# Kernel tuning notes

Measured on AMD Instinct MI355X. Metric: run time of the kernel, lower is better.

## Reference

```python
import jax, jax.numpy as jnp
import numpy as np

N_NODES = 50000
N_EDGES = 800000
N_GRAPHS = 500
DIM = 64
RBF_DIM = 5      # ceil(cutoff/width) = ceil(5.0/1)
N_CONV = 3
N_TYPES = 100
CLS_DIM = 2000
CUTOFF = 5.0

def _w(key, shape, fan_in):
    return jax.random.normal(key, shape, dtype=jnp.float32) / np.sqrt(fan_in)

def setup_inputs() -> dict:
    key = jax.random.key(0)
    ks = jax.random.split(key, 16)
    return {
        "node_types": jax.random.randint(ks[0], (N_NODES,), 0, N_TYPES, dtype=jnp.int32),
        "edge_src": jax.random.randint(ks[1], (N_EDGES,), 0, N_NODES, dtype=jnp.int32),
        "edge_dst": jax.random.randint(ks[2], (N_EDGES,), 0, N_NODES, dtype=jnp.int32),
        "graph_ids": jnp.sort(jax.random.randint(ks[3], (N_NODES,), 0, N_GRAPHS, dtype=jnp.int32)),
        "distance": jax.random.uniform(ks[4], (N_EDGES,), dtype=jnp.float32) * CUTOFF,
        "emb": jax.random.normal(ks[5], (N_TYPES, DIM), dtype=jnp.float32),
        "conv_w1": _w(ks[6], (N_CONV, DIM, DIM), DIM),
        "cf1_w": _w(ks[7], (N_CONV, RBF_DIM, DIM), RBF_DIM),
        "cf1_b": jnp.zeros((N_CONV, DIM), jnp.float32),
        "cf2_w": _w(ks[8], (N_CONV, DIM, DIM), DIM),
        "cf2_b": jnp.zeros((N_CONV, DIM), jnp.float32),
        "nl2_w": _w(ks[9], (N_CONV, DIM, DIM), DIM),
        "nl2_b": jnp.zeros((N_CONV, DIM), jnp.float32),
        "nl3_w": _w(ks[10], (N_CONV, DIM, DIM), DIM),
        "nl3_b": jnp.zeros((N_CONV, DIM), jnp.float32),
        "d1_w": _w(ks[11], (DIM, 256), DIM),
        "d1_b": jnp.zeros((256,), jnp.float32),
        "d2_w": _w(ks[12], (256, 256), 256),
        "d2_b": jnp.zeros((256,), jnp.float32),
        "cls_w": _w(ks[13], (256, CLS_DIM), 256),
        "cls_b": jnp.zeros((CLS_DIM,), jnp.float32),
        "ac_w": _w(ks[14], (256, N_TYPES), 256),
        "ac_b": jnp.zeros((N_TYPES,), jnp.float32),
    }

def _sp2(x):
    # torch nn.Softplus(beta=0.5): (1/0.5) * log(1 + exp(0.5 * x))
    return 2.0 * jax.nn.softplus(0.5 * x)

def reference(node_types, edge_src, edge_dst, graph_ids, distance, emb,
              conv_w1, cf1_w, cf1_b, cf2_w, cf2_b, nl2_w, nl2_b, nl3_w, nl3_b,
              d1_w, d1_b, d2_w, d2_b, cls_w, cls_b, ac_w, ac_b):
    # RBF expansion of edge distances: centers = linspace(low, high, n_centers)
    centers = jnp.linspace(0.0, CUTOFF, RBF_DIM)
    gap = centers[1] - centers[0]
    rbf = jnp.exp(-(1.0 / gap) * (distance[:, None] - centers) ** 2)  # [E, RBF_DIM]

    node = emb[node_types]                                            # AtomEmbedding -> [N, D]
    for i in range(N_CONV):                                           # Interaction layers
        new_node = node @ conv_w1[i]                                  # Linear(dim, dim, bias=False)
        eh = _sp2(rbf @ cf1_w[i] + cf1_b[i])                          # CFConv filter network
        eh = _sp2(eh @ cf2_w[i] + cf2_b[i])                           # [E, D]
        msg = new_node[edge_src] * eh                                 # fn.u_mul_e gather
        agg = jax.ops.segment_sum(msg, edge_dst, num_segments=N_NODES)  # fn.sum scatter
        t = _sp2(agg @ nl2_w[i] + nl2_b[i])
        node = node + t @ nl3_w[i] + nl3_b[i]                         # residual update

    atom = node @ d1_w + d1_b
    atom = jax.nn.softplus(atom) - jnp.log(2.0)                       # ShiftSoftplus
    res = atom @ d2_w + d2_b                                          # [N, 256]
    atoms_preds = jax.nn.relu(res) @ ac_w + ac_b                      # [N, 100]

    ones = jnp.ones((N_NODES,), jnp.float32)
    counts = jax.ops.segment_sum(ones, graph_ids, num_segments=N_GRAPHS)
    emb_g = jax.ops.segment_sum(res, graph_ids, num_segments=N_GRAPHS) / jnp.maximum(counts, 1.0)[:, None]
    cls_preds = emb_g @ cls_w + cls_b                                 # [B, cls_dim]
    return atoms_preds, cls_preds
```

## Files before the change

### kernel.cpp

```cpp
#include <hip/hip_runtime.h>
#include <math.h>

#define N_NODES 50000
#define N_EDGES 800000
#define N_GRAPHS 500
#define DIM 64
#define RBF_DIM 5
#define N_CONV 3
#define CLS_DIM 2000
#define ACT_DIM 100
#define HID 256
#define TAB 2048
#define CAP 64

typedef __attribute__((ext_vector_type(8))) short bf16x8;
typedef __attribute__((ext_vector_type(4))) float f32x4;
#define MFMA16(a,b,c) __builtin_amdgcn_mfma_f32_16x16x32_bf16(a,b,c,0,0,0)

__device__ __forceinline__ float sp2f(float x){
    float y = 0.5f * x;
    return 2.0f * (fmaxf(y, 0.0f) + log1pf(__expf(-fabsf(y))));
}
__device__ __forceinline__ float sspf(float x){
    return fmaxf(x, 0.0f) + log1pf(__expf(-fabsf(x))) - 0.69314718055994531f;
}
__device__ __forceinline__ short f2b(float x){
    union { float f; unsigned u; } v; v.f = x;
    unsigned r = v.u + 0x7FFFu + ((v.u >> 16) & 1u);
    return (short)(r >> 16);
}
__device__ __forceinline__ float b2f(short x){
    union { unsigned u; float f; } v; v.u = ((unsigned)(unsigned short)x) << 16;
    return v.f;
}

__global__ void k_tw(const float* __restrict__ cw, const float* __restrict__ n2,
                     const float* __restrict__ n3, const float* __restrict__ d1w,
                     const float* __restrict__ d2w, const float* __restrict__ acw,
                     const float* __restrict__ clsw, const float* __restrict__ emb,
                     short* __restrict__ cwt, short* __restrict__ n2t, short* __restrict__ n3t,
                     short* __restrict__ d1t, short* __restrict__ d2t, short* __restrict__ act,
                     short* __restrict__ clswt, short* __restrict__ embw0b){
    int b = blockIdx.x, tid = threadIdx.x;
    if (b < 144){
        int i = b * 256 + tid;
        int y = i >> 12, j = i & 4095;
        int which = y / 3, layer = y % 3;
        const float* src = (which == 0 ? cw : which == 1 ? n2 : n3) + layer * 4096;
        short* dst = (which == 0 ? cwt : which == 1 ? n2t : n3t) + layer * 4096;
        int k = j >> 6, n = j & 63;
        dst[n * 64 + k] = f2b(src[k * 64 + n]);
    } else if (b < 208){
        int i = (b - 144) * 256 + tid;
        int k = i >> 8, n = i & 255;
        d1t[n * 64 + k] = f2b(d1w[k * 256 + n]);
    } else if (b < 464){
        int i = (b - 208) * 256 + tid;
        int k = i >> 8, n = i & 255;
        d2t[n * 256 + k] = f2b(d2w[k * 256 + n]);
    } else if (b < 576){
        int i = (b - 464) * 256 + tid;
        int n = i >> 8, k = i & 255;
        act[n * 256 + k] = f2b(n < ACT_DIM ? acw[k * ACT_DIM + n] : 0.f);
    } else if (b < 2624){
        int i = (b - 576) * 256 + tid;
        int k = i >> 11, n = i & 2047;
        clswt[n * 256 + k] = f2b(n < CLS_DIM ? clsw[k * CLS_DIM + n] : 0.f);
    } else {
        int i = (b - 2624) * 256 + tid;
        if (i < 100 * 64){
            int t = i >> 6, c = i & 63;
            float a = 0.f;
            #pragma unroll 8
            for (int k = 0; k < 64; ++k) a += emb[t * 64 + k] * cw[k * 64 + c];
            embw0b[i] = f2b(a);
        }
    }
}

__global__ void k_embed(const int* __restrict__ types, const float* __restrict__ emb,
                        const short* __restrict__ embw0b,
                        float* __restrict__ node, short* __restrict__ nodeb,
                        short* __restrict__ nnb,
                        const int* __restrict__ gid, float* __restrict__ counts,
                        const int* __restrict__ esrc, const int* __restrict__ edst,
                        const float* __restrict__ dist,
                        int* __restrict__ cnt, unsigned* __restrict__ edata){
    int i = blockIdx.x * 256 + threadIdx.x;
    if (i < N_NODES * DIM){
        int t = types[i >> 6], c = i & 63;
        float v = emb[t * 64 + c];
        node[i] = v; nodeb[i] = f2b(v);
        nnb[i] = embw0b[t * 64 + c];
    }
    if (i < N_EDGES){
        int d = edst[i];
        int pos = atomicAdd(&cnt[d], 1);
        if (pos < CAP){
            const float SC16 = (float)(TAB - 1) * 16.0f / 5.0f;
            int v = (int)(dist[i] * SC16 + 0.5f);
            v = min(v, 32767);
            edata[pos * N_NODES + d] = ((unsigned)v << 17) | (unsigned)esrc[i];
        }
    }
    if (i < N_NODES) atomicAdd(&counts[gid[i]], 1.0f);
}

__global__ __launch_bounds__(256) void k_table3(const float* __restrict__ cf1w_all,
    const float* __restrict__ cf1b_all, const float* __restrict__ cf2w_all,
    const float* __restrict__ cf2b_all, short* __restrict__ tabb_all)
{
    int L = blockIdx.y;
    const float* cf1w = cf1w_all + L * RBF_DIM * DIM;
    const float* cf1b = cf1b_all + L * DIM;
    const float* cf2w = cf2w_all + L * DIM * DIM;
    const float* cf2b = cf2b_all + L * DIM;
    short* tabb = tabb_all + L * TAB * 64;
    __shared__ float s_cf1[RBF_DIM * 64];
    __shared__ float s_cf1b[64], s_cf2b[64];
    __shared__ float s_cf2[64 * 64];
    __shared__ float s_h1[4 * 64];
    int tid = threadIdx.x;
    int c = tid & 63, g = tid >> 6;
    for (int i = tid; i < 64 * 64; i += 256) s_cf2[i] = cf2w[i];
    for (int i = tid; i < RBF_DIM * 64; i += 256) s_cf1[i] = cf1w[i];
    if (tid < 64){ s_cf1b[tid] = cf1b[tid]; s_cf2b[tid] = cf2b[tid]; }
    __syncthreads();
    int entry = blockIdx.x * 4 + g;
    float d = (float)entry * (5.0f / (float)(TAB - 1));
    {
        float acc = s_cf1b[c];
        #pragma unroll
        for (int j = 0; j < RBF_DIM; ++j){
            float t = d - 1.25f * (float)j;
            acc += __expf(-0.8f * t * t) * s_cf1[j * 64 + c];
        }
        s_h1[g * 64 + c] = sp2f(acc);
    }
    __syncthreads();
    {
        float acc = s_cf2b[c];
        #pragma unroll 8
        for (int k = 0; k < 64; ++k) acc += s_h1[g * 64 + k] * s_cf2[k * 64 + c];
        tabb[entry * 64 + c] = f2b(sp2f(acc));
    }
}

__global__ void k_pack(const short* __restrict__ tabb_all, unsigned* __restrict__ tabp_all){
    int L = blockIdx.y;
    int i = blockIdx.x * 256 + threadIdx.x;
    if (i < (TAB - 1) * 64){
        int t = i >> 6, c = i & 63;
        unsigned lo = (unsigned short)tabb_all[L * TAB * 64 + t * 64 + c];
        unsigned hi = (unsigned short)tabb_all[L * TAB * 64 + (t + 1) * 64 + c];
        tabp_all[L * TAB * 64 + t * 64 + c] = lo | (hi << 16);
    }
}

__global__ __launch_bounds__(256) void k_agg(const unsigned* __restrict__ edata,
    const int* __restrict__ cnt, const unsigned* __restrict__ tabp,
    const short* __restrict__ nnb, short* __restrict__ aggb)
{
    int tid = threadIdx.x;
    int c = tid & 63, r = tid >> 6;
    int n = blockIdx.x * 4 + r;
    if (n >= N_NODES) return;
    int m = min(cnt[n], CAP);
    unsigned ev = (c < m) ? edata[(long)c * N_NODES + n] : 0u;
    int s_l = (int)(ev & 0x1FFFFu);
    int v_l = (int)(ev >> 17);
    int i0_l = min(v_l >> 4, TAB - 2);
    float f_l = (float)(v_l - (i0_l << 4)) * 0.0625f;
    int pk_l = (i0_l << 17) | s_l;
    float acc = 0.f;
    int e = 0;
    for (; e + 4 <= m; e += 4){
        int   pa = __shfl(pk_l, e);     float fa = __shfl(f_l, e);
        int   pb = __shfl(pk_l, e + 1); float fb = __shfl(f_l, e + 1);
        int   pc = __shfl(pk_l, e + 2); float fc = __shfl(f_l, e + 2);
        int   pd = __shfl(pk_l, e + 3); float fd = __shfl(f_l, e + 3);
        int ia = pa >> 17, sa = pa & 0x1FFFF;
        int ib = pb >> 17, sb = pb & 0x1FFFF;
        int ic = pc >> 17, sc = pc & 0x1FFFF;
        int id = pd >> 17, sd = pd & 0x1FFFF;
        unsigned ua = tabp[ia * 64 + c], ub = tabp[ib * 64 + c];
        unsigned uc = tabp[ic * 64 + c], ud = tabp[id * 64 + c];
        float na = b2f(nnb[sa * 64 + c]), nb = b2f(nnb[sb * 64 + c]);
        float nc = b2f(nnb[sc * 64 + c]), nd = b2f(nnb[sd * 64 + c]);
        float wa0 = __uint_as_float(ua << 16), wa1 = __uint_as_float(ua & 0xffff0000u);
        float wb0 = __uint_as_float(ub << 16), wb1 = __uint_as_float(ub & 0xffff0000u);
        float wc0 = __uint_as_float(uc << 16), wc1 = __uint_as_float(uc & 0xffff0000u);
        float wd0 = __uint_as_float(ud << 16), wd1 = __uint_as_float(ud & 0xffff0000u);
        acc += na * (wa0 + (wa1 - wa0) * fa);
        acc += nb * (wb0 + (wb1 - wb0) * fb);
        acc += nc * (wc0 + (wc1 - wc0) * fc);
        acc += nd * (wd0 + (wd1 - wd0) * fd);
    }
    for (; e < m; ++e){
        int   p = __shfl(pk_l, e); float f = __shfl(f_l, e);
        int i0 = p >> 17, s = p & 0x1FFFF;
        unsigned u = tabp[i0 * 64 + c];
        float w0 = __uint_as_float(u << 16), w1 = __uint_as_float(u & 0xffff0000u);
        acc += b2f(nnb[s * 64 + c]) * (w0 + (w1 - w0) * f);
    }
    aggb[n * 64 + c] = f2b(acc);
}

__global__ __launch_bounds__(256) void k_update(const short* __restrict__ aggb,
    const short* __restrict__ nl2t, const float* __restrict__ nl2b,
    const short* __restrict__ nl3t, const float* __restrict__ nl3b,
    float* __restrict__ node, short* __restrict__ nodeb,
    const short* __restrict__ wnext, short* __restrict__ nnb)
{
    __shared__ short sT[32 * 80];
    int tid = threadIdx.x, wave = tid >> 6, lane = tid & 63;
    int quad = lane >> 4, l16 = lane & 15;
    int row0 = blockIdx.x * 32;
    int rt = wave >> 1;
    int ctb = (wave & 1) * 2;
    f32x4 acc[2] = {{0,0,0,0},{0,0,0,0}};
    #pragma unroll
    for (int kt = 0; kt < 2; ++kt){
        int k0 = kt * 32 + quad * 8;
        int rw = row0 + rt * 16 + l16;
        bf16x8 a = (rw < N_NODES) ? *(const bf16x8*)&aggb[rw * 64 + k0] : (bf16x8){0,0,0,0,0,0,0,0};
        #pragma unroll
        for (int i = 0; i < 2; ++i){
            bf16x8 b = *(const bf16x8*)&nl2t[((ctb + i) * 16 + l16) * 64 + k0];
            acc[i] = MFMA16(a, b, acc[i]);
        }
    }
    #pragma unroll
    for (int i = 0; i < 2; ++i)
        #pragma unroll
        for (int reg = 0; reg < 4; ++reg){
            int rl = rt * 16 + quad * 4 + reg;
            int col = (ctb + i) * 16 + l16;
            sT[rl * 80 + col] = f2b(sp2f(acc[i][reg] + nl2b[col]));
        }
    __syncthreads();
    f32x4 acc2[2] = {{0,0,0,0},{0,0,0,0}};
    #pragma unroll
    for (int kt = 0; kt < 2; ++kt){
        int k0 = kt * 32 + quad * 8;
        bf16x8 a = *(const bf16x8*)&sT[(rt * 16 + l16) * 80 + k0];
        #pragma unroll
        for (int i = 0; i < 2; ++i){
            bf16x8 b = *(const bf16x8*)&nl3t[((ctb + i) * 16 + l16) * 64 + k0];
            acc2[i] = MFMA16(a, b, acc2[i]);
        }
    }
    short vb[2][4];
    #pragma unroll
    for (int i = 0; i < 2; ++i)
        #pragma unroll
        for (int reg = 0; reg < 4; ++reg){
            int row = row0 + rt * 16 + quad * 4 + reg;
            int col = (ctb + i) * 16 + l16;
            float v = 0.f;
            if (row < N_NODES){
                v = node[row * 64 + col] + acc2[i][reg] + nl3b[col];
                node[row * 64 + col] = v;
            }
            short vbs = f2b(v);
            vb[i][reg] = vbs;
            if (row < N_NODES) nodeb[row * 64 + col] = vbs;
        }
    if (wnext){
        __syncthreads();
        #pragma unroll
        for (int i = 0; i < 2; ++i)
            #pragma unroll
            for (int reg = 0; reg < 4; ++reg)
                sT[(rt * 16 + quad * 4 + reg) * 80 + (ctb + i) * 16 + l16] = vb[i][reg];
        __syncthreads();
        f32x4 acc3[2] = {{0,0,0,0},{0,0,0,0}};
        #pragma unroll
        for (int kt = 0; kt < 2; ++kt){
            int k0 = kt * 32 + quad * 8;
            bf16x8 a = *(const bf16x8*)&sT[(rt * 16 + l16) * 80 + k0];
            #pragma unroll
            for (int i = 0; i < 2; ++i){
                bf16x8 b = *(const bf16x8*)&wnext[((ctb + i) * 16 + l16) * 64 + k0];
                acc3[i] = MFMA16(a, b, acc3[i]);
            }
        }
        #pragma unroll
        for (int i = 0; i < 2; ++i)
            #pragma unroll
            for (int reg = 0; reg < 4; ++reg){
                int row = row0 + rt * 16 + quad * 4 + reg;
                int col = (ctb + i) * 16 + l16;
                if (row < N_NODES) nnb[row * 64 + col] = f2b(acc3[i][reg]);
            }
    }
}

__global__ __launch_bounds__(256) void k_r1(const short* __restrict__ nodeb,
    const short* __restrict__ d1t, const float* __restrict__ d1b,
    short* __restrict__ atomb)
{
    int tid = threadIdx.x, wave = tid >> 6, lane = tid & 63;
    int quad = lane >> 4, l16 = lane & 15;
    int row0 = blockIdx.x * 32;
    f32x4 acc[2][4] = {{{0,0,0,0},{0,0,0,0},{0,0,0,0},{0,0,0,0}},
                       {{0,0,0,0},{0,0,0,0},{0,0,0,0},{0,0,0,0}}};
    #pragma unroll
    for (int kt = 0; kt < 2; ++kt){
        int k0 = kt * 32 + quad * 8;
        bf16x8 a[2];
        #pragma unroll
        for (int rt = 0; rt < 2; ++rt){
            int rw = row0 + rt * 16 + l16;
            a[rt] = (rw < N_NODES) ? *(const bf16x8*)&nodeb[rw * 64 + k0] : (bf16x8){0,0,0,0,0,0,0,0};
        }
        #pragma unroll
        for (int ct = 0; ct < 4; ++ct){
            int n = wave * 64 + ct * 16 + l16;
            bf16x8 b = *(const bf16x8*)&d1t[n * 64 + k0];
            #pragma unroll
            for (int rt = 0; rt < 2; ++rt) acc[rt][ct] = MFMA16(a[rt], b, acc[rt][ct]);
        }
    }
    #pragma unroll
    for (int rt = 0; rt < 2; ++rt)
        #pragma unroll
        for (int ct = 0; ct < 4; ++ct){
            int col = wave * 64 + ct * 16 + l16;
            float bb = d1b[col];
            #pragma unroll
            for (int reg = 0; reg < 4; ++reg){
                int row = row0 + rt * 16 + quad * 4 + reg;
                if (row < N_NODES) atomb[row * HID + col] = f2b(sspf(acc[rt][ct][reg] + bb));
            }
        }
}

__global__ __launch_bounds__(256) void k_r2(const short* __restrict__ atomb,
    const short* __restrict__ d2t, const float* __restrict__ d2b_,
    const int* __restrict__ gid, float* __restrict__ gacc, short* __restrict__ resb)
{
    __shared__ float sres[32 * 260];
    int tid = threadIdx.x, wave = tid >> 6, lane = tid & 63;
    int quad = lane >> 4, l16 = lane & 15;
    int row0 = blockIdx.x * 32;
    f32x4 acc[2][4] = {{{0,0,0,0},{0,0,0,0},{0,0,0,0},{0,0,0,0}},
                       {{0,0,0,0},{0,0,0,0},{0,0,0,0},{0,0,0,0}}};
    for (int kt = 0; kt < 8; ++kt){
        int k0 = kt * 32 + quad * 8;
        bf16x8 a[2];
        #pragma unroll
        for (int rt = 0; rt < 2; ++rt){
            int rw = row0 + rt * 16 + l16;
            a[rt] = (rw < N_NODES) ? *(const bf16x8*)&atomb[rw * HID + k0] : (bf16x8){0,0,0,0,0,0,0,0};
        }
        #pragma unroll
        for (int ct = 0; ct < 4; ++ct){
            int n = wave * 64 + ct * 16 + l16;
            bf16x8 b = *(const bf16x8*)&d2t[n * HID + k0];
            #pragma unroll
            for (int rt = 0; rt < 2; ++rt) acc[rt][ct] = MFMA16(a[rt], b, acc[rt][ct]);
        }
    }
    #pragma unroll
    for (int rt = 0; rt < 2; ++rt)
        #pragma unroll
        for (int ct = 0; ct < 4; ++ct){
            int col = wave * 64 + ct * 16 + l16;
            float bb = d2b_[col];
            #pragma unroll
            for (int reg = 0; reg < 4; ++reg){
                int rl = rt * 16 + quad * 4 + reg;
                sres[rl * 260 + col] = acc[rt][ct][reg] + bb;
            }
        }
    __syncthreads();
    float run = 0.f; int cur = -1;
    for (int r = 0; r < 32; ++r){
        int n = row0 + r;
        if (n >= N_NODES) break;
        float v = sres[r * 260 + tid];
        int g = gid[n];
        if (g != cur){
            if (cur >= 0) atomicAdd(&gacc[cur * HID + tid], run);
            run = 0.f; cur = g;
        }
        run += v;
        resb[n * HID + tid] = f2b(fmaxf(v, 0.f));
    }
    if (cur >= 0) atomicAdd(&gacc[cur * HID + tid], run);
}

__global__ __launch_bounds__(256) void k_r3(const short* __restrict__ resb,
    const short* __restrict__ act, const float* __restrict__ acb,
    float* __restrict__ out_atoms)
{
    int tid = threadIdx.x, wave = tid >> 6, lane = tid & 63;
    int quad = lane >> 4, l16 = lane & 15;
    int row0 = blockIdx.x * 64;
    f32x4 acc[7] = {{0,0,0,0},{0,0,0,0},{0,0,0,0},{0,0,0,0},{0,0,0,0},{0,0,0,0},{0,0,0,0}};
    for (int kt = 0; kt < 8; ++kt){
        int k0 = kt * 32 + quad * 8;
        int rw = row0 + wave * 16 + l16;
        bf16x8 a = (rw < N_NODES) ? *(const bf16x8*)&resb[rw * HID + k0] : (bf16x8){0,0,0,0,0,0,0,0};
        #pragma unroll
        for (int ct = 0; ct < 7; ++ct){
            bf16x8 b = *(const bf16x8*)&act[(ct * 16 + l16) * HID + k0];
            acc[ct] = MFMA16(a, b, acc[ct]);
        }
    }
    #pragma unroll
    for (int ct = 0; ct < 7; ++ct){
        int col = ct * 16 + l16;
        if (col >= ACT_DIM) continue;
        float bb = acb[col];
        #pragma unroll
        for (int reg = 0; reg < 4; ++reg){
            int row = row0 + wave * 16 + quad * 4 + reg;
            if (row < N_NODES) out_atoms[row * ACT_DIM + col] = acc[ct][reg] + bb;
        }
    }
}

__global__ void k_embg(const float* __restrict__ gacc, const float* __restrict__ counts,
                       short* __restrict__ gclsb){
    int i = blockIdx.x * 256 + threadIdx.x;
    if (i < N_GRAPHS * HID){
        int g = i >> 8;
        gclsb[i] = f2b(gacc[i] / fmaxf(counts[g], 1.0f));
    }
}

__global__ __launch_bounds__(256) void k_cls2(const short* __restrict__ gclsb,
    const short* __restrict__ clswt, const float* __restrict__ clsb,
    float* __restrict__ out_cls)
{
    int tid = threadIdx.x, wave = tid >> 6, lane = tid & 63;
    int quad = lane >> 4, l16 = lane & 15;
    int row0 = blockIdx.x * 32;
    int colbase = blockIdx.y * 256 + wave * 64;
    f32x4 acc[2][4] = {{{0,0,0,0},{0,0,0,0},{0,0,0,0},{0,0,0,0}},
                       {{0,0,0,0},{0,0,0,0},{0,0,0,0},{0,0,0,0}}};
    for (int kt = 0; kt < 8; ++kt){
        int k0 = kt * 32 + quad * 8;
        bf16x8 a[2];
        #pragma unroll
        for (int rt = 0; rt < 2; ++rt){
            int rw = row0 + rt * 16 + l16;
            a[rt] = (rw < N_GRAPHS) ? *(const bf16x8*)&gclsb[rw * HID + k0] : (bf16x8){0,0,0,0,0,0,0,0};
        }
        #pragma unroll
        for (int ct = 0; ct < 4; ++ct){
            bf16x8 b = *(const bf16x8*)&clswt[(colbase + ct * 16 + l16) * HID + k0];
            #pragma unroll
            for (int rt = 0; rt < 2; ++rt) acc[rt][ct] = MFMA16(a[rt], b, acc[rt][ct]);
        }
    }
    #pragma unroll
    for (int rt = 0; rt < 2; ++rt)
        #pragma unroll
        for (int ct = 0; ct < 4; ++ct){
            int col = colbase + ct * 16 + l16;
            if (col >= CLS_DIM) continue;
            float bb = clsb[col];
            #pragma unroll
            for (int reg = 0; reg < 4; ++reg){
                int row = row0 + rt * 16 + quad * 4 + reg;
                if (row < N_GRAPHS) out_cls[row * CLS_DIM + col] = acc[rt][ct][reg] + bb;
            }
        }
}

extern "C" void kernel_launch(void* const* d_in, const int* in_sizes, int n_in,
                              void* d_out, int out_size, void* d_ws, size_t ws_size,
                              hipStream_t stream)
{
    const int*   node_types = (const int*)d_in[0];
    const int*   edge_src   = (const int*)d_in[1];
    const int*   edge_dst   = (const int*)d_in[2];
    const int*   graph_ids  = (const int*)d_in[3];
    const float* distance   = (const float*)d_in[4];
    const float* emb        = (const float*)d_in[5];
    const float* conv_w1    = (const float*)d_in[6];
    const float* cf1_w      = (const float*)d_in[7];
    const float* cf1_b      = (const float*)d_in[8];
    const float* cf2_w      = (const float*)d_in[9];
    const float* cf2_b      = (const float*)d_in[10];
    const float* nl2_w      = (const float*)d_in[11];
    const float* nl2_b      = (const float*)d_in[12];
    const float* nl3_w      = (const float*)d_in[13];
    const float* nl3_b      = (const float*)d_in[14];
    const float* d1_w       = (const float*)d_in[15];
    const float* d1_b       = (const float*)d_in[16];
    const float* d2_w       = (const float*)d_in[17];
    const float* d2_b       = (const float*)d_in[18];
    const float* cls_w      = (const float*)d_in[19];
    const float* cls_b      = (const float*)d_in[20];
    const float* ac_w       = (const float*)d_in[21];
    const float* ac_b       = (const float*)d_in[22];

    float*    gacc   = (float*)d_ws;
    float*    counts = gacc + 128000;
    int*      cnt    = (int*)(counts + 512);
    short*    nodeb  = (short*)(cnt + 50048);
    short*    nnb    = nodeb + 3200000;
    short*    aggb   = nnb + 3200000;
    short*    tabb   = aggb + 3200000;
    unsigned* tabp   = (unsigned*)(tabb + 3 * 131072);
    short*    cw1t   = (short*)(tabp + 3 * 131072);
    short*    n2t    = cw1t + 12288;
    short*    n3t    = n2t + 12288;
    short*    d1t    = n3t + 12288;
    short*    d2t    = d1t + 16384;
    short*    act    = d2t + 65536;
    short*    clswt  = act + 28672;
    short*    gclsb  = clswt + 524288;
    short*    embw0b = gclsb + 128000;
    float*    node   = (float*)(embw0b + 6400);
    unsigned* edata  = (unsigned*)(node + 3200000);
    short*    atomb  = (short*)node;
    short*    resb   = atomb;
    float*    out    = (float*)d_out;

    (void)hipMemsetAsync(gacc, 0, (128000 + 512) * sizeof(float) + 50048 * sizeof(int), stream);

    k_tw<<<2649, 256, 0, stream>>>(conv_w1, nl2_w, nl3_w, d1_w, d2_w, ac_w, cls_w, emb,
                                   cw1t, n2t, n3t, d1t, d2t, act, clswt, embw0b);
    k_table3<<<dim3(TAB / 4, 3), 256, 0, stream>>>(cf1_w, cf1_b, cf2_w, cf2_b, tabb);
    k_pack<<<dim3(512, 3), 256, 0, stream>>>(tabb, tabp);

    k_embed<<<(N_NODES * DIM + 255) / 256, 256, 0, stream>>>(node_types, emb, embw0b,
        node, nodeb, nnb, graph_ids, counts, edge_src, edge_dst, distance, cnt, edata);

    for (int i = 0; i < N_CONV; ++i){
        k_agg<<<(N_NODES + 3) / 4, 256, 0, stream>>>(edata, cnt, tabp + i * TAB * 64,
                                                     nnb, aggb);
        k_update<<<(N_NODES + 31) / 32, 256, 0, stream>>>(aggb,
            n2t + i * 4096, nl2_b + i * DIM, n3t + i * 4096, nl3_b + i * DIM,
            node, nodeb, (i < N_CONV - 1) ? (cw1t + (i + 1) * 4096) : (const short*)nullptr, nnb);
    }

    k_r1<<<(N_NODES + 31) / 32, 256, 0, stream>>>(nodeb, d1t, d1_b, atomb);
    k_r2<<<(N_NODES + 31) / 32, 256, 0, stream>>>(atomb, d2t, d2_b, graph_ids, gacc, resb);
    k_r3<<<(N_NODES + 63) / 64, 256, 0, stream>>>(resb, act, ac_b, out);
    k_embg<<<(N_GRAPHS * HID + 255) / 256, 256, 0, stream>>>(gacc, counts, gclsb);
    k_cls2<<<dim3((N_GRAPHS + 31) / 32, (CLS_DIM + 255) / 256), 256, 0, stream>>>(
        gclsb, clswt, cls_b, out + N_NODES * ACT_DIM);
}
```

Measured before the change: 495.9 us.

## Shrink filter table to 256 entries, stage it in LDS, use node-major edge layout

The precomputed edge-filter table shrinks from 2048 to 256 interpolation points. Each k_agg block (now 1024 threads covering 16 nodes) copies the packed table for the current layer into shared memory, and table lookups read LDS instead of global memory. k_table3 now writes the packed lo/hi pairs directly, which removes the k_pack kernel. Edge bucketing moves into a separate k_scat kernel that stores each node's edge list contiguously, and the coarser table adds interpolation error to the filter values.

```diff
diff --git a/kernel.cpp b/kernel.cpp
--- a/kernel.cpp
+++ b/kernel.cpp
@@ -10,7 +10,8 @@
 #define CLS_DIM 2000
 #define ACT_DIM 100
 #define HID 256
-#define TAB 2048
+#define TAB 256
+#define TABP (TAB - 1)
 #define CAP 64
 
 typedef __attribute__((ext_vector_type(8))) short bf16x8;
@@ -82,10 +83,7 @@
                         const short* __restrict__ embw0b,
                         float* __restrict__ node, short* __restrict__ nodeb,
                         short* __restrict__ nnb,
-                        const int* __restrict__ gid, float* __restrict__ counts,
-                        const int* __restrict__ esrc, const int* __restrict__ edst,
-                        const float* __restrict__ dist,
-                        int* __restrict__ cnt, unsigned* __restrict__ edata){
+                        const int* __restrict__ gid, float* __restrict__ counts){
     int i = blockIdx.x * 256 + threadIdx.x;
     if (i < N_NODES * DIM){
         int t = types[i >> 6], c = i & 63;
@@ -93,29 +91,34 @@
         node[i] = v; nodeb[i] = f2b(v);
         nnb[i] = embw0b[t * 64 + c];
     }
-    if (i < N_EDGES){
-        int d = edst[i];
-        int pos = atomicAdd(&cnt[d], 1);
-        if (pos < CAP){
-            const float SC16 = (float)(TAB - 1) * 16.0f / 5.0f;
-            int v = (int)(dist[i] * SC16 + 0.5f);
-            v = min(v, 32767);
-            edata[pos * N_NODES + d] = ((unsigned)v << 17) | (unsigned)esrc[i];
-        }
-    }
     if (i < N_NODES) atomicAdd(&counts[gid[i]], 1.0f);
+}
+
+__global__ void k_scat(const int* __restrict__ esrc, const int* __restrict__ edst,
+                       const float* __restrict__ dist,
+                       int* __restrict__ cnt, unsigned* __restrict__ edata){
+    int e = blockIdx.x * 256 + threadIdx.x;
+    if (e >= N_EDGES) return;
+    int d = edst[e];
+    int pos = atomicAdd(&cnt[d], 1);
+    if (pos < CAP){
+        const float SC16 = (float)(TAB - 1) * 16.0f / 5.0f;
+        int v = (int)(dist[e] * SC16 + 0.5f);
+        v = min(v, (TAB - 1) * 16);
+        edata[d * CAP + pos] = ((unsigned)v << 17) | (unsigned)esrc[e];
+    }
 }
 
 __global__ __launch_bounds__(256) void k_table3(const float* __restrict__ cf1w_all,
     const float* __restrict__ cf1b_all, const float* __restrict__ cf2w_all,
-    const float* __restrict__ cf2b_all, short* __restrict__ tabb_all)
+    const float* __restrict__ cf2b_all, unsigned* __restrict__ tabp_all)
 {
     int L = blockIdx.y;
     const float* cf1w = cf1w_all + L * RBF_DIM * DIM;
     const float* cf1b = cf1b_all + L * DIM;
     const float* cf2w = cf2w_all + L * DIM * DIM;
     const float* cf2b = cf2b_all + L * DIM;
-    short* tabb = tabb_all + L * TAB * 64;
+    unsigned short* tp = (unsigned short*)(tabp_all + L * TABP * 64);
     __shared__ float s_cf1[RBF_DIM * 64];
     __shared__ float s_cf1b[64], s_cf2b[64];
     __shared__ float s_cf2[64 * 64];
@@ -142,31 +145,24 @@
         float acc = s_cf2b[c];
         #pragma unroll 8
         for (int k = 0; k < 64; ++k) acc += s_h1[g * 64 + k] * s_cf2[k * 64 + c];
-        tabb[entry * 64 + c] = f2b(sp2f(acc));
-    }
-}
-
-__global__ void k_pack(const short* __restrict__ tabb_all, unsigned* __restrict__ tabp_all){
-    int L = blockIdx.y;
-    int i = blockIdx.x * 256 + threadIdx.x;
-    if (i < (TAB - 1) * 64){
-        int t = i >> 6, c = i & 63;
-        unsigned lo = (unsigned short)tabb_all[L * TAB * 64 + t * 64 + c];
-        unsigned hi = (unsigned short)tabb_all[L * TAB * 64 + (t + 1) * 64 + c];
-        tabp_all[L * TAB * 64 + t * 64 + c] = lo | (hi << 16);
-    }
-}
-
-__global__ __launch_bounds__(256) void k_agg(const unsigned* __restrict__ edata,
+        unsigned short h = (unsigned short)f2b(sp2f(acc));
+        if (entry < TABP) tp[(entry * 64 + c) * 2] = h;
+        if (entry > 0)    tp[((entry - 1) * 64 + c) * 2 + 1] = h;
+    }
+}
+
+__global__ __launch_bounds__(1024) void k_agg(const unsigned* __restrict__ edata,
     const int* __restrict__ cnt, const unsigned* __restrict__ tabp,
     const short* __restrict__ nnb, short* __restrict__ aggb)
 {
+    __shared__ unsigned s_tab[TABP * 64];
     int tid = threadIdx.x;
+    for (int i = tid; i < TABP * 64; i += 1024) s_tab[i] = tabp[i];
+    __syncthreads();
     int c = tid & 63, r = tid >> 6;
-    int n = blockIdx.x * 4 + r;
-    if (n >= N_NODES) return;
+    int n = blockIdx.x * 16 + r;
     int m = min(cnt[n], CAP);
-    unsigned ev = (c < m) ? edata[(long)c * N_NODES + n] : 0u;
+    unsigned ev = (c < m) ? edata[n * CAP + c] : 0u;
     int s_l = (int)(ev & 0x1FFFFu);
     int v_l = (int)(ev >> 17);
     int i0_l = min(v_l >> 4, TAB - 2);
@@ -183,8 +179,8 @@
         int ib = pb >> 17, sb = pb & 0x1FFFF;
         int ic = pc >> 17, sc = pc & 0x1FFFF;
         int id = pd >> 17, sd = pd & 0x1FFFF;
-        unsigned ua = tabp[ia * 64 + c], ub = tabp[ib * 64 + c];
-        unsigned uc = tabp[ic * 64 + c], ud = tabp[id * 64 + c];
+        unsigned ua = s_tab[ia * 64 + c], ub = s_tab[ib * 64 + c];
+        unsigned uc = s_tab[ic * 64 + c], ud = s_tab[id * 64 + c];
         float na = b2f(nnb[sa * 64 + c]), nb = b2f(nnb[sb * 64 + c]);
         float nc = b2f(nnb[sc * 64 + c]), nd = b2f(nnb[sd * 64 + c]);
         float wa0 = __uint_as_float(ua << 16), wa1 = __uint_as_float(ua & 0xffff0000u);
@@ -199,7 +195,7 @@
     for (; e < m; ++e){
         int   p = __shfl(pk_l, e); float f = __shfl(f_l, e);
         int i0 = p >> 17, s = p & 0x1FFFF;
-        unsigned u = tabp[i0 * 64 + c];
+        unsigned u = s_tab[i0 * 64 + c];
         float w0 = __uint_as_float(u << 16), w1 = __uint_as_float(u & 0xffff0000u);
         acc += b2f(nnb[s * 64 + c]) * (w0 + (w1 - w0) * f);
     }
@@ -505,9 +501,8 @@
     short*    nodeb  = (short*)(cnt + 50048);
     short*    nnb    = nodeb + 3200000;
     short*    aggb   = nnb + 3200000;
-    short*    tabb   = aggb + 3200000;
-    unsigned* tabp   = (unsigned*)(tabb + 3 * 131072);
-    short*    cw1t   = (short*)(tabp + 3 * 131072);
+    unsigned* tabp   = (unsigned*)(aggb + 3200000);
+    short*    cw1t   = (short*)(tabp + 3 * 16320);
     short*    n2t    = cw1t + 12288;
     short*    n3t    = n2t + 12288;
     short*    d1t    = n3t + 12288;
@@ -526,15 +521,16 @@
 
     k_tw<<<2649, 256, 0, stream>>>(conv_w1, nl2_w, nl3_w, d1_w, d2_w, ac_w, cls_w, emb,
                                    cw1t, n2t, n3t, d1t, d2t, act, clswt, embw0b);
-    k_table3<<<dim3(TAB / 4, 3), 256, 0, stream>>>(cf1_w, cf1_b, cf2_w, cf2_b, tabb);
-    k_pack<<<dim3(512, 3), 256, 0, stream>>>(tabb, tabp);
+    k_table3<<<dim3(TAB / 4, 3), 256, 0, stream>>>(cf1_w, cf1_b, cf2_w, cf2_b, tabp);
 
     k_embed<<<(N_NODES * DIM + 255) / 256, 256, 0, stream>>>(node_types, emb, embw0b,
-        node, nodeb, nnb, graph_ids, counts, edge_src, edge_dst, distance, cnt, edata);
+        node, nodeb, nnb, graph_ids, counts);
+    k_scat<<<(N_EDGES + 255) / 256, 256, 0, stream>>>(edge_src, edge_dst, distance,
+                                                      cnt, edata);
 
     for (int i = 0; i < N_CONV; ++i){
-        k_agg<<<(N_NODES + 3) / 4, 256, 0, stream>>>(edata, cnt, tabp + i * TAB * 64,
-                                                     nnb, aggb);
+        k_agg<<<N_NODES / 16, 1024, 0, stream>>>(edata, cnt, tabp + i * TABP * 64,
+                                                 nnb, aggb);
         k_update<<<(N_NODES + 31) / 32, 256, 0, stream>>>(aggb,
             n2t + i * 4096, nl2_b + i * DIM, n3t + i * 4096, nl3_b + i * DIM,
             node, nodeb, (i < N_CONV - 1) ? (cw1t + (i + 1) * 4096) : (const short*)nullptr, nnb);
```

After: 549.6 us. +10.8%, slower.
